# Optimization experiments

Hardware: AMD Instinct MI355X
Metric: run time of the kernel (lower is better)

Reference implementation:

```python
import jax, jax.numpy as jnp
import numpy as np

N_NODES = 50000
N_EDGES = 800000
NUM_GRAPHS = 64
EPS = 1e-5


def setup_inputs() -> dict:
    key = jax.random.key(0)
    ks = jax.random.split(key, 24)
    d = {}
    d['x'] = jax.random.normal(ks[0], (N_NODES, 128), dtype=jnp.float32)
    d['edge_index'] = jax.random.randint(ks[1], (2, N_EDGES), 0, N_NODES, dtype=jnp.int32)
    d['batch'] = jnp.sort(jax.random.randint(ks[2], (N_NODES,), 0, NUM_GRAPHS, dtype=jnp.int32))
    def w(k, shape, fan_in):
        return jax.random.normal(k, shape, dtype=jnp.float32) * (1.0 / np.sqrt(fan_in))
    d['W1'] = w(ks[3], (128, 256), 128)
    d['asrc1'] = w(ks[4], (4, 64), 64)
    d['adst1'] = w(ks[5], (4, 64), 64)
    d['b1'] = jnp.zeros((256,), jnp.float32)
    d['g1'] = jnp.ones((256,), jnp.float32)
    d['be1'] = jnp.zeros((256,), jnp.float32)
    d['W2'] = w(ks[6], (256, 256), 256)
    d['asrc2'] = w(ks[7], (4, 64), 64)
    d['adst2'] = w(ks[8], (4, 64), 64)
    d['b2'] = jnp.zeros((256,), jnp.float32)
    d['g2'] = jnp.ones((256,), jnp.float32)
    d['be2'] = jnp.zeros((256,), jnp.float32)
    d['W3'] = w(ks[9], (256, 128), 256)
    d['asrc3'] = w(ks[10], (1, 128), 128)
    d['adst3'] = w(ks[11], (1, 128), 128)
    d['b3'] = jnp.zeros((128,), jnp.float32)
    d['g3'] = jnp.ones((128,), jnp.float32)
    d['be3'] = jnp.zeros((128,), jnp.float32)
    d['Wp'] = w(ks[12], (256, 128), 256)
    d['bp'] = jnp.zeros((128,), jnp.float32)
    return d


def _gat(x, src, dst, W, a_src, a_dst, b, concat):
    # PyG GATConv: shared linear, per-edge additive attention, segment softmax over dst
    N = x.shape[0]
    H, C = a_src.shape
    xl = (x @ W).reshape(N, H, C)                       # [N,H,C]
    a_l = jnp.sum(xl * a_src[None], axis=-1)            # [N,H]
    a_r = jnp.sum(xl * a_dst[None], axis=-1)            # [N,H]
    e = jax.nn.leaky_relu(a_l[src] + a_r[dst], 0.2)     # [E,H]
    m = jax.ops.segment_max(e, dst, num_segments=N)
    m = jnp.where(jnp.isfinite(m), m, 0.0)
    p = jnp.exp(e - m[dst])
    s = jax.ops.segment_sum(p, dst, num_segments=N)
    alpha = p / (s[dst] + 1e-16)                        # [E,H]
    out = jax.ops.segment_sum(alpha[:, :, None] * xl[src], dst, num_segments=N)  # [N,H,C]
    out = out.reshape(N, H * C) if concat else out.mean(axis=1)
    return out + b


def _ln(x, g, b):
    mu = x.mean(-1, keepdims=True)
    var = x.var(-1, keepdims=True)
    return (x - mu) * jax.lax.rsqrt(var + EPS) * g + b


def reference(x, edge_index, batch, W1, asrc1, adst1, b1, g1, be1,
              W2, asrc2, adst2, b2, g2, be2,
              W3, asrc3, adst3, b3, g3, be3, Wp, bp):
    N = x.shape[0]
    loops = jnp.arange(N, dtype=edge_index.dtype)
    src = jnp.concatenate([edge_index[0], loops])  # add_self_loops=True
    dst = jnp.concatenate([edge_index[1], loops])
    h = jax.nn.relu(_ln(_gat(x, src, dst, W1, asrc1, adst1, b1, True), g1, be1))
    h = jax.nn.relu(_ln(_gat(h, src, dst, W2, asrc2, adst2, b2, True), g2, be2))
    h = jax.nn.relu(_ln(_gat(h, src, dst, W3, asrc3, adst3, b3, False), g3, be3))
    cnt = jax.ops.segment_sum(jnp.ones((N,), h.dtype), batch, num_segments=NUM_GRAPHS)
    h_mean = jax.ops.segment_sum(h, batch, num_segments=NUM_GRAPHS) / jnp.maximum(cnt, 1.0)[:, None]
    h_max = jax.ops.segment_max(h, batch, num_segments=NUM_GRAPHS)
    g = jnp.concatenate([h_mean, h_max], axis=-1)       # [B, 2*embed]
    return g @ Wp + bp
```

## Files before the change

kernel.cpp:

```cpp
#include <hip/hip_runtime.h>

#define EPS_LN 1e-5f
typedef unsigned int uint;

using bf16x8 = __attribute__((ext_vector_type(8))) short;
using f32x4  = __attribute__((ext_vector_type(4))) float;

__device__ inline float bf2f(ushort h){ return __uint_as_float(((uint)h) << 16); }
__device__ inline ushort f2bf(float f){
  uint u = __float_as_uint(f);
  u += 0x7fffu + ((u >> 16) & 1u);
  return (ushort)(u >> 16);
}

__device__ inline void gload_lds16(const ushort* g, ushort* l){
  __builtin_amdgcn_global_load_lds(
      (const __attribute__((address_space(1))) uint*)g,
      (__attribute__((address_space(3))) uint*)l, 16, 0, 0);
}

#define POOL_Q 32

__global__ void k_deg(const int* __restrict__ ei, int* __restrict__ deg, int E, int N){
  int e = blockIdx.x * 256 + threadIdx.x;
  if (e >= E + N) return;
  int dst = (e < E) ? ei[E + e] : (e - E);
  atomicAdd(&deg[dst], 1);
}

__global__ __launch_bounds__(1024) void k_bsum(const int* __restrict__ deg, int* __restrict__ bsum, int n){
  __shared__ int ws[16];
  const int t = (int)threadIdx.x, lane = t & 63, w = t >> 6;
  int i = blockIdx.x * 1024 + t;
  int v = (i < n) ? deg[i] : 0;
  #pragma unroll
  for (int off = 32; off; off >>= 1) v += __shfl_xor(v, off);
  if (lane == 0) ws[w] = v;
  __syncthreads();
  if (t == 0){
    int s = 0;
    #pragma unroll
    for (int k = 0; k < 16; k++) s += ws[k];
    bsum[blockIdx.x] = s;
  }
}

__global__ __launch_bounds__(256) void k_misc(int* __restrict__ bsum, int nb,
                                              const int* __restrict__ batch, int* __restrict__ pos,
                                              float* __restrict__ pool_sum, uint* __restrict__ pool_max,
                                              int N, int G){
  const int t = (int)threadIdx.x;
  const int b = (int)blockIdx.x;
  if (b == 0){
    if (t >= 64) return;
    const int lane = t;
    int carry = 0;
    for (int b0 = 0; b0 < nb; b0 += 64){
      int i = b0 + lane;
      int v = (i < nb) ? bsum[i] : 0;
      int s = v;
      #pragma unroll
      for (int off = 1; off < 64; off <<= 1){ int u = __shfl_up(s, off); if (lane >= off) s += u; }
      if (i < nb) bsum[i] = s - v + carry;
      carry += __shfl(s, 63);
    }
  } else if (b == 1){
    int g = t;
    if (g > G) return;
    int lo = 0, hi = N;
    while (lo < hi){
      int mid = (lo + hi) >> 1;
      if (batch[mid] < g) lo = mid + 1; else hi = mid;
    }
    pos[g] = lo;
  } else {
    int i = (b - 2) * 256 + t;
    if (i < G * 128){ pool_sum[i] = 0.f; pool_max[i] = 0u; }
  }
}

__global__ __launch_bounds__(1024) void k_scan2(const int* __restrict__ deg, const int* __restrict__ bpre,
                                                int* __restrict__ row_ptr, int* __restrict__ cursor, int n){
  __shared__ int wsum[16];
  const int t = (int)threadIdx.x, lane = t & 63, w = t >> 6;
  int i = blockIdx.x * 1024 + t;
  int v = (i < n) ? deg[i] : 0;
  int s = v;
  #pragma unroll
  for (int off = 1; off < 64; off <<= 1){ int u = __shfl_up(s, off); if (lane >= off) s += u; }
  if (lane == 63) wsum[w] = s;
  __syncthreads();
  if (w == 0 && lane < 16){
    int sc = wsum[lane];
    #pragma unroll
    for (int off = 1; off < 16; off <<= 1){ int u = __shfl_up(sc, off); if (lane >= off) sc += u; }
    wsum[lane] = sc;
  }
  __syncthreads();
  int prefix = bpre[blockIdx.x] + (w ? wsum[w - 1] : 0) + s;
  if (i < n){ row_ptr[i + 1] = prefix; cursor[i] = prefix - v; }
  if (i == 0) row_ptr[0] = 0;
}

__global__ void k_scatter(const int* __restrict__ ei, int* __restrict__ cursor,
                          int* __restrict__ csr_src, int E, int N){
  int e = blockIdx.x * 256 + threadIdx.x;
  if (e >= E + N) return;
  int src, dst;
  if (e < E){ src = ei[e]; dst = ei[E + e]; } else { src = dst = e - E; }
  int pos = atomicAdd(&cursor[dst], 1);
  csr_src[pos] = src;
}

__global__ void k_prep(const float* __restrict__ x, ushort* __restrict__ x_bf,
                       const float* __restrict__ W1, ushort* __restrict__ W1t,
                       const float* __restrict__ W2, ushort* __restrict__ W2t,
                       const float* __restrict__ W3, ushort* __restrict__ W3t, int N){
  int i = blockIdx.x * 256 + threadIdx.x;
  const int c0 = N * 32;
  if (i < c0){
    float4 v = reinterpret_cast<const float4*>(x)[i];
    ushort4 o; o.x = f2bf(v.x); o.y = f2bf(v.y); o.z = f2bf(v.z); o.w = f2bf(v.w);
    reinterpret_cast<ushort4*>(x_bf)[i] = o;
    return;
  }
  i -= c0;
  if (i < 256 * 128){
    int n = i >> 7, k = i & 127;
    W1t[i] = f2bf(W1[(size_t)k * 256 + n]);
    return;
  }
  i -= 256 * 128;
  if (i < 256 * 256){
    int n = i >> 8, k = i & 255;
    W2t[i] = f2bf(W2[(size_t)k * 256 + n]);
    return;
  }
  i -= 256 * 256;
  if (i < 128 * 256){
    int n = i >> 8, k = i & 255;
    W3t[i] = f2bf(W3[(size_t)k * 128 + n]);
  }
}

template<int K, int N, int H>
__global__ __launch_bounds__(256, 4) void k_mm(const ushort* __restrict__ A,
                                               const ushort* __restrict__ Wt,
                                               ushort* __restrict__ out,
                                               const float* __restrict__ asrc,
                                               const float* __restrict__ adst,
                                               float* __restrict__ al, float* __restrict__ ar,
                                               int M)
{
  constexpr int BANDS = (N / H) / 64;
  __shared__ __align__(16) ushort ldsA[128 * 64];
  __shared__ __align__(16) ushort ldsB[128 * 64];

  const int t = (int)threadIdx.x;
  const int lane = t & 63;
  const int w = t >> 6;
  const int wm = w >> 1, wn = w & 1;
  const int row0 = blockIdx.x * 128;
  const int n0 = blockIdx.y * 128;
  const int growR = w * 8 + (lane >> 3);
  const int gcolA = (lane & 7) * 8;

  f32x4 acc[4][4];
  #pragma unroll
  for (int mt = 0; mt < 4; mt++)
    #pragma unroll
    for (int nt = 0; nt < 4; nt++)
      acc[mt][nt] = (f32x4){0.f, 0.f, 0.f, 0.f};

  #pragma unroll
  for (int kt = 0; kt < K / 64; kt++){
    if (kt) __syncthreads();
    #pragma unroll
    for (int r = 0; r < 4; r++){
      int ga = row0 + r * 32 + growR; if (ga > M - 1) ga = M - 1;
      int gb = n0 + r * 32 + growR;
      gload_lds16(&A [(size_t)ga * K + kt * 64 + gcolA], ldsA + r * 2048 + w * 512);
      gload_lds16(&Wt[(size_t)gb * K + kt * 64 + gcolA], ldsB + r * 2048 + w * 512);
    }
    __syncthreads();

    #pragma unroll
    for (int ks = 0; ks < 2; ks++){
      bf16x8 af[4], bfr[4];
      const int kb8 = ks * 4 + (lane >> 4);
      #pragma unroll
      for (int mt = 0; mt < 4; mt++){
        int arow = wm * 64 + mt * 16 + (lane & 15);
        af[mt]  = *reinterpret_cast<const bf16x8*>(&ldsA[arow * 64 + kb8 * 8]);
        int brow = wn * 64 + mt * 16 + (lane & 15);
        bfr[mt] = *reinterpret_cast<const bf16x8*>(&ldsB[brow * 64 + kb8 * 8]);
      }
      #pragma unroll
      for (int mt = 0; mt < 4; mt++)
        #pragma unroll
        for (int nt = 0; nt < 4; nt++)
          acc[mt][nt] = __builtin_amdgcn_mfma_f32_16x16x32_bf16(af[mt], bfr[nt], acc[mt][nt], 0, 0, 0);
    }
  }

  #pragma unroll
  for (int mt = 0; mt < 4; mt++){
    const int grow_b = row0 + wm * 64 + mt * 16 + (lane >> 4) * 4;
    #pragma unroll
    for (int nt = 0; nt < 4; nt++){
      const int gcol = n0 + wn * 64 + nt * 16 + (lane & 15);
      #pragma unroll
      for (int r = 0; r < 4; r++){
        int grow = grow_b + r;
        if (grow < M) out[(size_t)grow * N + gcol] = f2bf(acc[mt][nt][r]);
      }
    }
  }

  float av[4], bv[4];
  #pragma unroll
  for (int nt = 0; nt < 4; nt++){
    int col = n0 + wn * 64 + nt * 16 + (lane & 15);
    av[nt] = asrc[col]; bv[nt] = adst[col];
  }
  float paA[4][4], pbA[4][4];
  #pragma unroll
  for (int mt = 0; mt < 4; mt++){
    #pragma unroll
    for (int r = 0; r < 4; r++){
      float pa = acc[mt][0][r] * av[0] + acc[mt][1][r] * av[1]
               + acc[mt][2][r] * av[2] + acc[mt][3][r] * av[3];
      float pb = acc[mt][0][r] * bv[0] + acc[mt][1][r] * bv[1]
               + acc[mt][2][r] * bv[2] + acc[mt][3][r] * bv[3];
      #pragma unroll
      for (int off = 1; off < 16; off <<= 1){ pa += __shfl_xor(pa, off); pb += __shfl_xor(pb, off); }
      paA[mt][r] = pa; pbA[mt][r] = pb;
    }
  }
  if constexpr (BANDS == 1){
    const int h = (n0 + wn * 64) / (N / H);
    if ((lane & 15) == 0){
      #pragma unroll
      for (int mt = 0; mt < 4; mt++){
        #pragma unroll
        for (int r = 0; r < 4; r++){
          int row = row0 + wm * 64 + mt * 16 + (lane >> 4) * 4 + r;
          if (row < M){
            al[(size_t)row * H + h] = paA[mt][r];
            ar[(size_t)row * H + h] = pbA[mt][r];
          }
        }
      }
    }
  } else {
    __syncthreads();
    float* fl = reinterpret_cast<float*>(ldsA);
    if (wn == 0 && (lane & 15) == 0){
      #pragma unroll
      for (int mt = 0; mt < 4; mt++){
        #pragma unroll
        for (int r = 0; r < 4; r++){
          int rl = wm * 64 + mt * 16 + (lane >> 4) * 4 + r;
          fl[rl] = paA[mt][r]; fl[128 + rl] = pbA[mt][r];
        }
      }
    }
    __syncthreads();
    if (wn == 1 && (lane & 15) == 0){
      #pragma unroll
      for (int mt = 0; mt < 4; mt++){
        #pragma unroll
        for (int r = 0; r < 4; r++){
          int rl = wm * 64 + mt * 16 + (lane >> 4) * 4 + r;
          int row = row0 + rl;
          if (row < M){
            al[row] = fl[rl] + paA[mt][r];
            ar[row] = fl[128 + rl] + pbA[mt][r];
          }
        }
      }
    }
  }
}

template<int DIM>
__device__ inline void gstep4(const char* __restrict__ xlb, int laneB, int s, float p, float* acc){
  uint2 v = *reinterpret_cast<const uint2*>(xlb + (size_t)((uint)s * (uint)(DIM * 2)) + laneB);
  acc[0] = fmaf(p, __uint_as_float(v.x << 16), acc[0]);
  acc[1] = fmaf(p, __uint_as_float(v.x & 0xffff0000u), acc[1]);
  acc[2] = fmaf(p, __uint_as_float(v.y << 16), acc[2]);
  acc[3] = fmaf(p, __uint_as_float(v.y & 0xffff0000u), acc[3]);
}
template<int DIM>
__device__ inline void gstep2(const char* __restrict__ xlb, int laneB, int s, float p, float* acc){
  uint v = *reinterpret_cast<const uint*>(xlb + (size_t)((uint)s * (uint)(DIM * 2)) + laneB);
  acc[0] = fmaf(p, __uint_as_float(v << 16), acc[0]);
  acc[1] = fmaf(p, __uint_as_float(v & 0xffff0000u), acc[1]);
}

template<int H, int DIM, bool BF16_OUT>
__global__ __launch_bounds__(256) void k_aggw(
    const ushort* __restrict__ xl,
    const float* __restrict__ al, const float* __restrict__ ar,
    const int* __restrict__ row_ptr, const int* __restrict__ csr_src,
    const float* __restrict__ bias, const float* __restrict__ gamma, const float* __restrict__ beta,
    float* __restrict__ out, int N)
{
  constexpr int EPL = DIM / 64;
  constexpr int PST = 68;
  const int tid = (int)threadIdx.x;
  const int wid = tid >> 6, lane = tid & 63;
  __shared__ float plds_all[4][H * PST];
  __shared__ int   slds_all[4][64];
  float* plds = plds_all[wid];
  int*   slds = slds_all[wid];
  const int n = blockIdx.x * 4 + wid;
  if (n >= N) return;
  const int start = __builtin_amdgcn_readfirstlane(row_ptr[n]);
  const int end   = __builtin_amdgcn_readfirstlane(row_ptr[n + 1]);
  const int deg   = end - start;
  const int hm    = (H == 4) ? (lane >> 4) : 0;
  const int hb    = hm * PST;
  const int laneB = lane * (EPL * 2);

  float arv[H];
  #pragma unroll
  for (int h = 0; h < H; h++) arv[h] = ar[(size_t)n * H + h];

  float acc[EPL];
  #pragma unroll
  for (int e = 0; e < EPL; e++) acc[e] = 0.f;
  float psum[H];
  const char* xlb = (const char*)xl;

  auto gather = [&](int cnt){
    int j = 0;
    for (; j + 8 <= cnt; j += 8){
      int s0 = slds[j+0], s1 = slds[j+1], s2 = slds[j+2], s3 = slds[j+3];
      int s4 = slds[j+4], s5 = slds[j+5], s6 = slds[j+6], s7 = slds[j+7];
      float q0 = plds[hb+j+0], q1 = plds[hb+j+1], q2 = plds[hb+j+2], q3 = plds[hb+j+3];
      float q4 = plds[hb+j+4], q5 = plds[hb+j+5], q6 = plds[hb+j+6], q7 = plds[hb+j+7];
      if constexpr (EPL == 4){
        gstep4<DIM>(xlb, laneB, s0, q0, acc); gstep4<DIM>(xlb, laneB, s1, q1, acc);
        gstep4<DIM>(xlb, laneB, s2, q2, acc); gstep4<DIM>(xlb, laneB, s3, q3, acc);
        gstep4<DIM>(xlb, laneB, s4, q4, acc); gstep4<DIM>(xlb, laneB, s5, q5, acc);
        gstep4<DIM>(xlb, laneB, s6, q6, acc); gstep4<DIM>(xlb, laneB, s7, q7, acc);
      } else {
        gstep2<DIM>(xlb, laneB, s0, q0, acc); gstep2<DIM>(xlb, laneB, s1, q1, acc);
        gstep2<DIM>(xlb, laneB, s2, q2, acc); gstep2<DIM>(xlb, laneB, s3, q3, acc);
        gstep2<DIM>(xlb, laneB, s4, q4, acc); gstep2<DIM>(xlb, laneB, s5, q5, acc);
        gstep2<DIM>(xlb, laneB, s6, q6, acc); gstep2<DIM>(xlb, laneB, s7, q7, acc);
      }
    }
    for (; j + 2 <= cnt; j += 2){
      int s0 = slds[j+0], s1 = slds[j+1];
      float q0 = plds[hb+j+0], q1 = plds[hb+j+1];
      if constexpr (EPL == 4){ gstep4<DIM>(xlb, laneB, s0, q0, acc); gstep4<DIM>(xlb, laneB, s1, q1, acc); }
      else                   { gstep2<DIM>(xlb, laneB, s0, q0, acc); gstep2<DIM>(xlb, laneB, s1, q1, acc); }
    }
    if (j < cnt){
      int s0 = slds[j];
      float q0 = plds[hb+j];
      if constexpr (EPL == 4) gstep4<DIM>(xlb, laneB, s0, q0, acc);
      else                    gstep2<DIM>(xlb, laneB, s0, q0, acc);
    }
  };

  if (deg <= 64){
    int src = csr_src[start + (lane < deg ? lane : deg - 1)];
    slds[lane] = src;
    float e[H];
    if constexpr (H == 4){
      float4 a4 = *reinterpret_cast<const float4*>(&al[(size_t)src * 4]);
      e[0] = a4.x + arv[0]; e[1] = a4.y + arv[1]; e[2] = a4.z + arv[2]; e[3] = a4.w + arv[3];
    } else {
      e[0] = al[src] + arv[0];
    }
    #pragma unroll
    for (int h = 0; h < H; h++){
      e[h] = e[h] > 0.f ? e[h] : 0.2f * e[h];
      if (lane >= deg) e[h] = -1e30f;
    }
    float mx[H];
    #pragma unroll
    for (int h = 0; h < H; h++){
      mx[h] = e[h];
      #pragma unroll
      for (int off = 32; off; off >>= 1) mx[h] = fmaxf(mx[h], __shfl_xor(mx[h], off));
    }
    #pragma unroll
    for (int h = 0; h < H; h++){
      float p = (lane < deg) ? __expf(e[h] - mx[h]) : 0.f;
      plds[h * PST + lane] = p;
      psum[h] = p;
      #pragma unroll
      for (int off = 32; off; off >>= 1) psum[h] += __shfl_xor(psum[h], off);
    }
    __asm__ volatile("s_waitcnt lgkmcnt(0)" ::: "memory");
    __builtin_amdgcn_wave_barrier();
    gather(deg);
  } else {
    float mx[H];
    #pragma unroll
    for (int h = 0; h < H; h++) mx[h] = -1e30f;
    for (int i = start + lane; i < end; i += 64){
      int src = csr_src[i];
      if constexpr (H == 4){
        float4 a4 = *reinterpret_cast<const float4*>(&al[(size_t)src * 4]);
        float e0 = a4.x + arv[0]; e0 = e0 > 0.f ? e0 : 0.2f * e0; mx[0] = fmaxf(mx[0], e0);
        float e1 = a4.y + arv[1]; e1 = e1 > 0.f ? e1 : 0.2f * e1; mx[1] = fmaxf(mx[1], e1);
        float e2 = a4.z + arv[2]; e2 = e2 > 0.f ? e2 : 0.2f * e2; mx[2] = fmaxf(mx[2], e2);
        float e3 = a4.w + arv[3]; e3 = e3 > 0.f ? e3 : 0.2f * e3; mx[3] = fmaxf(mx[3], e3);
      } else {
        float e = al[src] + arv[0]; e = e > 0.f ? e : 0.2f * e; mx[0] = fmaxf(mx[0], e);
      }
    }
    #pragma unroll
    for (int h = 0; h < H; h++){
      #pragma unroll
      for (int off = 32; off; off >>= 1) mx[h] = fmaxf(mx[h], __shfl_xor(mx[h], off));
    }
    #pragma unroll
    for (int h = 0; h < H; h++) psum[h] = 0.f;
    for (int c0 = start; c0 < end; c0 += 64){
      const int cnt = min(64, end - c0);
      __asm__ volatile("s_waitcnt lgkmcnt(0)" ::: "memory");
      __builtin_amdgcn_wave_barrier();
      if (lane < cnt){
        int src = csr_src[c0 + lane];
        slds[lane] = src;
        if constexpr (H == 4){
          float4 a4 = *reinterpret_cast<const float4*>(&al[(size_t)src * 4]);
          float e0 = a4.x + arv[0]; e0 = e0 > 0.f ? e0 : 0.2f * e0; float p0 = __expf(e0 - mx[0]);
          float e1 = a4.y + arv[1]; e1 = e1 > 0.f ? e1 : 0.2f * e1; float p1 = __expf(e1 - mx[1]);
          float e2 = a4.z + arv[2]; e2 = e2 > 0.f ? e2 : 0.2f * e2; float p2 = __expf(e2 - mx[2]);
          float e3 = a4.w + arv[3]; e3 = e3 > 0.f ? e3 : 0.2f * e3; float p3 = __expf(e3 - mx[3]);
          plds[0 * PST + lane] = p0; plds[1 * PST + lane] = p1;
          plds[2 * PST + lane] = p2; plds[3 * PST + lane] = p3;
          psum[0] += p0; psum[1] += p1; psum[2] += p2; psum[3] += p3;
        } else {
          float e = al[src] + arv[0]; e = e > 0.f ? e : 0.2f * e; float p = __expf(e - mx[0]);
          plds[lane] = p; psum[0] += p;
        }
      }
      __asm__ volatile("s_waitcnt lgkmcnt(0)" ::: "memory");
      __builtin_amdgcn_wave_barrier();
      gather(cnt);
    }
    #pragma unroll
    for (int h = 0; h < H; h++){
      #pragma unroll
      for (int off = 32; off; off >>= 1) psum[h] += __shfl_xor(psum[h], off);
    }
  }

  float ssel;
  if constexpr (H == 4){
    ssel = (hm == 0) ? psum[0] : (hm == 1) ? psum[1] : (hm == 2) ? psum[2] : psum[3];
  } else {
    ssel = psum[0];
  }
  const float inv = 1.f / (ssel + 1e-16f);

  float v[EPL];
  if constexpr (EPL == 4){
    float4 bb = *reinterpret_cast<const float4*>(&bias[lane * 4]);
    v[0] = fmaf(acc[0], inv, bb.x); v[1] = fmaf(acc[1], inv, bb.y);
    v[2] = fmaf(acc[2], inv, bb.z); v[3] = fmaf(acc[3], inv, bb.w);
  } else {
    float2 bb = *reinterpret_cast<const float2*>(&bias[lane * 2]);
    v[0] = fmaf(acc[0], inv, bb.x); v[1] = fmaf(acc[1], inv, bb.y);
  }
  float s1 = 0.f, s2 = 0.f;
  #pragma unroll
  for (int e = 0; e < EPL; e++){ s1 += v[e]; s2 += v[e] * v[e]; }
  #pragma unroll
  for (int off = 32; off; off >>= 1){ s1 += __shfl_xor(s1, off); s2 += __shfl_xor(s2, off); }
  const float mu = s1 / DIM;
  const float rstd = rsqrtf(s2 / DIM - mu * mu + EPS_LN);

  if constexpr (EPL == 4){
    float4 gg = *reinterpret_cast<const float4*>(&gamma[lane * 4]);
    float4 be = *reinterpret_cast<const float4*>(&beta[lane * 4]);
    float o0 = fmaxf((v[0] - mu) * rstd * gg.x + be.x, 0.f);
    float o1 = fmaxf((v[1] - mu) * rstd * gg.y + be.y, 0.f);
    float o2 = fmaxf((v[2] - mu) * rstd * gg.z + be.z, 0.f);
    float o3 = fmaxf((v[3] - mu) * rstd * gg.w + be.w, 0.f);
    if constexpr (BF16_OUT){
      uint2 pk;
      pk.x = (uint)f2bf(o0) | ((uint)f2bf(o1) << 16);
      pk.y = (uint)f2bf(o2) | ((uint)f2bf(o3) << 16);
      *reinterpret_cast<uint2*>(&reinterpret_cast<ushort*>(out)[(size_t)n * DIM + lane * 4]) = pk;
    } else {
      *reinterpret_cast<float4*>(&out[(size_t)n * DIM + lane * 4]) = make_float4(o0, o1, o2, o3);
    }
  } else {
    float2 gg = *reinterpret_cast<const float2*>(&gamma[lane * 2]);
    float2 be = *reinterpret_cast<const float2*>(&beta[lane * 2]);
    float o0 = fmaxf((v[0] - mu) * rstd * gg.x + be.x, 0.f);
    float o1 = fmaxf((v[1] - mu) * rstd * gg.y + be.y, 0.f);
    if constexpr (BF16_OUT){
      uint pk = (uint)f2bf(o0) | ((uint)f2bf(o1) << 16);
      reinterpret_cast<uint*>(out)[(size_t)n * (DIM / 2) + lane] = pk;
    } else {
      *reinterpret_cast<float2*>(&out[(size_t)n * DIM + lane * 2]) = make_float2(o0, o1);
    }
  }
}

__global__ __launch_bounds__(256) void k_pool(const float* __restrict__ h, const int* __restrict__ pos,
    float* __restrict__ pool_sum, uint* __restrict__ pool_max){
  const int t = (int)threadIdx.x;
  const int g = blockIdx.x / POOL_Q;
  const int q = blockIdx.x % POOL_Q;
  const int s = pos[g], e = pos[g + 1];
  const int len = e - s;
  if (len <= 0) return;
  const int chunk = (len + POOL_Q - 1) / POOL_Q;
  const int n0 = s + q * chunk;
  const int n1 = min(n0 + chunk, e);
  if (n0 >= n1) return;
  const int qd = t & 31;
  const int slot = t >> 5;
  const int wid = t >> 6;

  float4 sum = make_float4(0.f, 0.f, 0.f, 0.f);
  float4 mx  = make_float4(0.f, 0.f, 0.f, 0.f);
  for (int n = n0 + slot; n < n1; n += 8){
    float4 v = *reinterpret_cast<const float4*>(&h[(size_t)n * 128 + qd * 4]);
    sum.x += v.x; sum.y += v.y; sum.z += v.z; sum.w += v.w;
    mx.x = fmaxf(mx.x, v.x); mx.y = fmaxf(mx.y, v.y);
    mx.z = fmaxf(mx.z, v.z); mx.w = fmaxf(mx.w, v.w);
  }
  sum.x += __shfl_xor(sum.x, 32); sum.y += __shfl_xor(sum.y, 32);
  sum.z += __shfl_xor(sum.z, 32); sum.w += __shfl_xor(sum.w, 32);
  mx.x = fmaxf(mx.x, __shfl_xor(mx.x, 32)); mx.y = fmaxf(mx.y, __shfl_xor(mx.y, 32));
  mx.z = fmaxf(mx.z, __shfl_xor(mx.z, 32)); mx.w = fmaxf(mx.w, __shfl_xor(mx.w, 32));
  __shared__ float4 lsum[4][32], lmax[4][32];
  if ((t & 63) < 32){ lsum[wid][qd] = sum; lmax[wid][qd] = mx; }
  __syncthreads();
  if (t < 32){
    float4 S = lsum[0][t], M = lmax[0][t];
    #pragma unroll
    for (int w = 1; w < 4; w++){
      float4 S2 = lsum[w][t], M2 = lmax[w][t];
      S.x += S2.x; S.y += S2.y; S.z += S2.z; S.w += S2.w;
      M.x = fmaxf(M.x, M2.x); M.y = fmaxf(M.y, M2.y);
      M.z = fmaxf(M.z, M2.z); M.w = fmaxf(M.w, M2.w);
    }
    float* ps = &pool_sum[g * 128 + t * 4];
    uint*  pm = &pool_max[g * 128 + t * 4];
    atomicAdd(&ps[0], S.x); atomicAdd(&ps[1], S.y);
    atomicAdd(&ps[2], S.z); atomicAdd(&ps[3], S.w);
    atomicMax(&pm[0], __float_as_uint(M.x)); atomicMax(&pm[1], __float_as_uint(M.y));
    atomicMax(&pm[2], __float_as_uint(M.z)); atomicMax(&pm[3], __float_as_uint(M.w));
  }
}

__global__ __launch_bounds__(128) void k_final(const float* __restrict__ pool_sum,
    const uint* __restrict__ pool_max, const int* __restrict__ pos,
    const float* __restrict__ Wp, const float* __restrict__ bp, float* __restrict__ out){
  const int g = blockIdx.x;
  const int j = (int)threadIdx.x;
  float inv = 1.f / fmaxf((float)(pos[g + 1] - pos[g]), 1.f);
  float acc = bp[j];
  #pragma unroll 4
  for (int k = 0; k < 128; k++)
    acc = fmaf(pool_sum[g * 128 + k] * inv, Wp[k * 128 + j], acc);
  #pragma unroll 4
  for (int k = 0; k < 128; k++)
    acc = fmaf(__uint_as_float(pool_max[g * 128 + k]), Wp[(128 + k) * 128 + j], acc);
  out[g * 128 + j] = acc;
}

extern "C" void kernel_launch(void* const* d_in, const int* in_sizes, int n_in,
                              void* d_out, int out_size, void* d_ws, size_t ws_size,
                              hipStream_t stream){
  const float* x     = (const float*)d_in[0];
  const int*   ei    = (const int*)d_in[1];
  const int*   batch = (const int*)d_in[2];
  const float* W1    = (const float*)d_in[3];
  const float* asrc1 = (const float*)d_in[4];
  const float* adst1 = (const float*)d_in[5];
  const float* b1    = (const float*)d_in[6];
  const float* g1    = (const float*)d_in[7];
  const float* be1   = (const float*)d_in[8];
  const float* W2    = (const float*)d_in[9];
  const float* asrc2 = (const float*)d_in[10];
  const float* adst2 = (const float*)d_in[11];
  const float* b2    = (const float*)d_in[12];
  const float* g2    = (const float*)d_in[13];
  const float* be2   = (const float*)d_in[14];
  const float* W3    = (const float*)d_in[15];
  const float* asrc3 = (const float*)d_in[16];
  const float* adst3 = (const float*)d_in[17];
  const float* b3    = (const float*)d_in[18];
  const float* g3    = (const float*)d_in[19];
  const float* be3   = (const float*)d_in[20];
  const float* Wp    = (const float*)d_in[21];
  const float* bp    = (const float*)d_in[22];

  const int N = in_sizes[0] / 128;
  const int E = in_sizes[1] / 2;
  const int G = out_size / 128;
  const int EN = E + N;

  char* ws = (char*)d_ws;
  size_t off = 0;
  auto alloc = [&](size_t bytes) -> char* {
    char* p = ws + off;
    off = (off + bytes + 255) & ~(size_t)255;
    return p;
  };
  ushort*   region0  = (ushort*)alloc((size_t)N * 256 * 2);
  ushort*   x_bf     = region0;
  ushort*   h_bf     = region0;
  ushort*   xbufA    = (ushort*)alloc((size_t)N * 256 * 2);
  float*    xbufB    = (float*)alloc((size_t)N * 128 * 4);
  float*    al       = (float*)alloc((size_t)N * 4 * 4);
  float*    ar       = (float*)alloc((size_t)N * 4 * 4);
  int*      deg      = (int*)alloc((size_t)N * 4);
  int*      row_ptr  = (int*)alloc((size_t)(N + 1) * 4);
  int*      cursor   = (int*)alloc((size_t)N * 4);
  int*      csr_src  = (int*)alloc((size_t)EN * 4);
  int*      pos      = (int*)alloc((size_t)(G + 1) * 4);
  float*    pool_sum = (float*)alloc((size_t)G * 128 * 4);
  uint*     pool_max = (uint*)alloc((size_t)G * 128 * 4);
  ushort*   W1t      = (ushort*)alloc((size_t)256 * 128 * 2);
  ushort*   W2t      = (ushort*)alloc((size_t)256 * 256 * 2);
  ushort*   W3t      = (ushort*)alloc((size_t)128 * 256 * 2);
  const int NB = (N + 1023) / 1024;
  int*      bsum     = (int*)alloc((size_t)NB * 4);

  hipMemsetAsync(deg, 0, (size_t)N * 4, stream);

  k_deg<<<(EN + 255) / 256, 256, 0, stream>>>(ei, deg, E, N);
  k_bsum<<<NB, 1024, 0, stream>>>(deg, bsum, N);
  k_misc<<<2 + (G * 128 + 255) / 256, 256, 0, stream>>>(bsum, NB, batch, pos, pool_sum, pool_max, N, G);
  k_scan2<<<NB, 1024, 0, stream>>>(deg, bsum, row_ptr, cursor, N);
  k_scatter<<<(EN + 255) / 256, 256, 0, stream>>>(ei, cursor, csr_src, E, N);
  {
    int total = N * 32 + 256 * 128 + 256 * 256 + 128 * 256;
    k_prep<<<(total + 255) / 256, 256, 0, stream>>>(x, x_bf, W1, W1t, W2, W2t, W3, W3t, N);
  }

  const int MB = (N + 127) / 128;
  const int NB4 = (N + 3) / 4;

  k_mm<128, 256, 4><<<dim3(MB, 2), 256, 0, stream>>>(x_bf, W1t, xbufA, asrc1, adst1, al, ar, N);
  k_aggw<4, 256, true><<<NB4, 256, 0, stream>>>(xbufA, al, ar, row_ptr, csr_src, b1, g1, be1, (float*)h_bf, N);

  k_mm<256, 256, 4><<<dim3(MB, 2), 256, 0, stream>>>(h_bf, W2t, xbufA, asrc2, adst2, al, ar, N);
  k_aggw<4, 256, true><<<NB4, 256, 0, stream>>>(xbufA, al, ar, row_ptr, csr_src, b2, g2, be2, (float*)h_bf, N);

  k_mm<256, 128, 1><<<dim3(MB, 1), 256, 0, stream>>>(h_bf, W3t, xbufA, asrc3, adst3, al, ar, N);
  k_aggw<1, 128, false><<<NB4, 256, 0, stream>>>(xbufA, al, ar, row_ptr, csr_src, b3, g3, be3, xbufB, N);

  k_pool<<<G * POOL_Q, 256, 0, stream>>>(xbufB, pos, pool_sum, pool_max);
  k_final<<<G, 128, 0, stream>>>(pool_sum, pool_max, pos, Wp, bp, (float*)d_out);
}
```

Before: 380.0 us.

## Use 512-thread full-width GEMM tiles and fold degree counting into prep kernel

Adds a k_mm8 kernel in which one 512-thread block computes all 256 output columns for 128 rows. The A tile is loaded once instead of once per column-half block, and each wave writes its head's attention logits directly. The degree atomics move into k_prep, which removes one kernel launch. Costs are higher LDS use per block (48 KB), lower occupancy, and atomic traffic mixed into the conversion kernel.

```diff
diff --git a/kernel.cpp b/kernel.cpp
--- a/kernel.cpp
+++ b/kernel.cpp
@@ -20,13 +20,6 @@
 }
 
 #define POOL_Q 32
-
-__global__ void k_deg(const int* __restrict__ ei, int* __restrict__ deg, int E, int N){
-  int e = blockIdx.x * 256 + threadIdx.x;
-  if (e >= E + N) return;
-  int dst = (e < E) ? ei[E + e] : (e - E);
-  atomicAdd(&deg[dst], 1);
-}
 
 __global__ __launch_bounds__(1024) void k_bsum(const int* __restrict__ deg, int* __restrict__ bsum, int n){
   __shared__ int ws[16];
@@ -115,7 +108,9 @@
 __global__ void k_prep(const float* __restrict__ x, ushort* __restrict__ x_bf,
                        const float* __restrict__ W1, ushort* __restrict__ W1t,
                        const float* __restrict__ W2, ushort* __restrict__ W2t,
-                       const float* __restrict__ W3, ushort* __restrict__ W3t, int N){
+                       const float* __restrict__ W3, ushort* __restrict__ W3t,
+                       const int* __restrict__ ei, int* __restrict__ deg,
+                       int N, int E){
   int i = blockIdx.x * 256 + threadIdx.x;
   const int c0 = N * 32;
   if (i < c0){
@@ -140,6 +135,114 @@
   if (i < 128 * 256){
     int n = i >> 8, k = i & 255;
     W3t[i] = f2bf(W3[(size_t)k * 128 + n]);
+    return;
+  }
+  i -= 128 * 256;
+  if (i < E + N){
+    int dst = (i < E) ? ei[E + i] : (i - E);
+    atomicAdd(&deg[dst], 1);
+  }
+}
+
+template<int K>
+__global__ __launch_bounds__(512, 2) void k_mm8(const ushort* __restrict__ A,
+                                                const ushort* __restrict__ Wt,
+                                                ushort* __restrict__ out,
+                                                const float* __restrict__ asrc,
+                                                const float* __restrict__ adst,
+                                                float* __restrict__ al, float* __restrict__ ar,
+                                                int M)
+{
+  __shared__ __align__(16) ushort ldsA[128 * 64];
+  __shared__ __align__(16) ushort ldsB[256 * 64];
+
+  const int t = (int)threadIdx.x;
+  const int lane = t & 63;
+  const int w = t >> 6;
+  const int wm = w >> 2, wn = w & 3;
+  const int row0 = blockIdx.x * 128;
+  const int rr = t >> 3;
+  const int gcolA = (t & 7) * 8;
+
+  f32x4 acc[4][4];
+  #pragma unroll
+  for (int mt = 0; mt < 4; mt++)
+    #pragma unroll
+    for (int nt = 0; nt < 4; nt++)
+      acc[mt][nt] = (f32x4){0.f, 0.f, 0.f, 0.f};
+
+  #pragma unroll
+  for (int kt = 0; kt < K / 64; kt++){
+    if (kt) __syncthreads();
+    #pragma unroll
+    for (int r = 0; r < 2; r++){
+      int ga = row0 + r * 64 + rr; if (ga > M - 1) ga = M - 1;
+      gload_lds16(&A[(size_t)ga * K + kt * 64 + gcolA], ldsA + r * 4096 + w * 512);
+    }
+    #pragma unroll
+    for (int r = 0; r < 4; r++){
+      int gb = r * 64 + rr;
+      gload_lds16(&Wt[(size_t)gb * K + kt * 64 + gcolA], ldsB + r * 4096 + w * 512);
+    }
+    __syncthreads();
+
+    #pragma unroll
+    for (int ks = 0; ks < 2; ks++){
+      bf16x8 af[4], bfr[4];
+      const int kb8 = ks * 4 + (lane >> 4);
+      #pragma unroll
+      for (int mt = 0; mt < 4; mt++){
+        int arow = wm * 64 + mt * 16 + (lane & 15);
+        af[mt]  = *reinterpret_cast<const bf16x8*>(&ldsA[arow * 64 + kb8 * 8]);
+        int brow = wn * 64 + mt * 16 + (lane & 15);
+        bfr[mt] = *reinterpret_cast<const bf16x8*>(&ldsB[brow * 64 + kb8 * 8]);
+      }
+      #pragma unroll
+      for (int mt = 0; mt < 4; mt++)
+        #pragma unroll
+        for (int nt = 0; nt < 4; nt++)
+          acc[mt][nt] = __builtin_amdgcn_mfma_f32_16x16x32_bf16(af[mt], bfr[nt], acc[mt][nt], 0, 0, 0);
+    }
+  }
+
+  #pragma unroll
+  for (int mt = 0; mt < 4; mt++){
+    const int grow_b = row0 + wm * 64 + mt * 16 + (lane >> 4) * 4;
+    #pragma unroll
+    for (int nt = 0; nt < 4; nt++){
+      const int gcol = wn * 64 + nt * 16 + (lane & 15);
+      #pragma unroll
+      for (int r = 0; r < 4; r++){
+        int grow = grow_b + r;
+        if (grow < M) out[(size_t)grow * 256 + gcol] = f2bf(acc[mt][nt][r]);
+      }
+    }
+  }
+
+  float av[4], bv[4];
+  #pragma unroll
+  for (int nt = 0; nt < 4; nt++){
+    int col = wn * 64 + nt * 16 + (lane & 15);
+    av[nt] = asrc[col]; bv[nt] = adst[col];
+  }
+  #pragma unroll
+  for (int mt = 0; mt < 4; mt++){
+    #pragma unroll
+    for (int r = 0; r < 4; r++){
+      float pa = acc[mt][0][r] * av[0] + acc[mt][1][r] * av[1]
+               + acc[mt][2][r] * av[2] + acc[mt][3][r] * av[3];
+      float pb = acc[mt][0][r] * bv[0] + acc[mt][1][r] * bv[1]
+               + acc[mt][2][r] * bv[2] + acc[mt][3][r] * bv[3];
+      #pragma unroll
+      for (int off = 1; off < 16; off <<= 1){ pa += __shfl_xor(pa, off); pb += __shfl_xor(pb, off); }
+      if ((lane & 15) == 0){
+        int row = row0 + wm * 64 + mt * 16 + (lane >> 4) * 4 + r;
+        if (row < M){
+          al[(size_t)row * 4 + wn] = pa;
+          ar[(size_t)row * 4 + wn] = pb;
+        }
+      }
+    }
   }
 }
 
@@ -152,7 +255,6 @@
                                                float* __restrict__ al, float* __restrict__ ar,
                                                int M)
 {
-  constexpr int BANDS = (N / H) / 64;
   __shared__ __align__(16) ushort ldsA[128 * 64];
   __shared__ __align__(16) ushort ldsB[128 * 64];
 
@@ -161,7 +263,6 @@
   const int w = t >> 6;
   const int wm = w >> 1, wn = w & 1;
   const int row0 = blockIdx.x * 128;
-  const int n0 = blockIdx.y * 128;
   const int growR = w * 8 + (lane >> 3);
   const int gcolA = (lane & 7) * 8;
 
@@ -178,7 +279,7 @@
     #pragma unroll
     for (int r = 0; r < 4; r++){
       int ga = row0 + r * 32 + growR; if (ga > M - 1) ga = M - 1;
-      int gb = n0 + r * 32 + growR;
+      int gb = r * 32 + growR;
       gload_lds16(&A [(size_t)ga * K + kt * 64 + gcolA], ldsA + r * 2048 + w * 512);
       gload_lds16(&Wt[(size_t)gb * K + kt * 64 + gcolA], ldsB + r * 2048 + w * 512);
     }
@@ -208,7 +309,7 @@
     const int grow_b = row0 + wm * 64 + mt * 16 + (lane >> 4) * 4;
     #pragma unroll
     for (int nt = 0; nt < 4; nt++){
-      const int gcol = n0 + wn * 64 + nt * 16 + (lane & 15);
+      const int gcol = wn * 64 + nt * 16 + (lane & 15);
       #pragma unroll
       for (int r = 0; r < 4; r++){
         int grow = grow_b + r;
@@ -220,7 +321,7 @@
   float av[4], bv[4];
   #pragma unroll
   for (int nt = 0; nt < 4; nt++){
-    int col = n0 + wn * 64 + nt * 16 + (lane & 15);
+    int col = wn * 64 + nt * 16 + (lane & 15);
     av[nt] = asrc[col]; bv[nt] = adst[col];
   }
   float paA[4][4], pbA[4][4];
@@ -237,46 +338,29 @@
       paA[mt][r] = pa; pbA[mt][r] = pb;
     }
   }
-  if constexpr (BANDS == 1){
-    const int h = (n0 + wn * 64) / (N / H);
-    if ((lane & 15) == 0){
-      #pragma unroll
-      for (int mt = 0; mt < 4; mt++){
-        #pragma unroll
-        for (int r = 0; r < 4; r++){
-          int row = row0 + wm * 64 + mt * 16 + (lane >> 4) * 4 + r;
-          if (row < M){
-            al[(size_t)row * H + h] = paA[mt][r];
-            ar[(size_t)row * H + h] = pbA[mt][r];
-          }
-        }
-      }
-    }
-  } else {
-    __syncthreads();
-    float* fl = reinterpret_cast<float*>(ldsA);
-    if (wn == 0 && (lane & 15) == 0){
-      #pragma unroll
-      for (int mt = 0; mt < 4; mt++){
-        #pragma unroll
-        for (int r = 0; r < 4; r++){
-          int rl = wm * 64 + mt * 16 + (lane >> 4) * 4 + r;
-          fl[rl] = paA[mt][r]; fl[128 + rl] = pbA[mt][r];
-        }
-      }
-    }
-    __syncthreads();
-    if (wn == 1 && (lane & 15) == 0){
-      #pragma unroll
-      for (int mt = 0; mt < 4; mt++){
-        #pragma unroll
-        for (int r = 0; r < 4; r++){
-          int rl = wm * 64 + mt * 16 + (lane >> 4) * 4 + r;
-          int row = row0 + rl;
-          if (row < M){
-            al[row] = fl[rl] + paA[mt][r];
-            ar[row] = fl[128 + rl] + pbA[mt][r];
-          }
+  __syncthreads();
+  float* fl = reinterpret_cast<float*>(ldsA);
+  if (wn == 0 && (lane & 15) == 0){
+    #pragma unroll
+    for (int mt = 0; mt < 4; mt++){
+      #pragma unroll
+      for (int r = 0; r < 4; r++){
+        int rl = wm * 64 + mt * 16 + (lane >> 4) * 4 + r;
+        fl[rl] = paA[mt][r]; fl[128 + rl] = pbA[mt][r];
+      }
+    }
+  }
+  __syncthreads();
+  if (wn == 1 && (lane & 15) == 0){
+    #pragma unroll
+    for (int mt = 0; mt < 4; mt++){
+      #pragma unroll
+      for (int r = 0; r < 4; r++){
+        int rl = wm * 64 + mt * 16 + (lane >> 4) * 4 + r;
+        int row = row0 + rl;
+        if (row < M){
+          al[row] = fl[rl] + paA[mt][r];
+          ar[row] = fl[128 + rl] + pbA[mt][r];
         }
       }
     }
@@ -634,26 +718,25 @@
 
   hipMemsetAsync(deg, 0, (size_t)N * 4, stream);
 
-  k_deg<<<(EN + 255) / 256, 256, 0, stream>>>(ei, deg, E, N);
+  {
+    int total = N * 32 + 256 * 128 + 256 * 256 + 128 * 256 + EN;
+    k_prep<<<(total + 255) / 256, 256, 0, stream>>>(x, x_bf, W1, W1t, W2, W2t, W3, W3t, ei, deg, N, E);
+  }
   k_bsum<<<NB, 1024, 0, stream>>>(deg, bsum, N);
   k_misc<<<2 + (G * 128 + 255) / 256, 256, 0, stream>>>(bsum, NB, batch, pos, pool_sum, pool_max, N, G);
   k_scan2<<<NB, 1024, 0, stream>>>(deg, bsum, row_ptr, cursor, N);
   k_scatter<<<(EN + 255) / 256, 256, 0, stream>>>(ei, cursor, csr_src, E, N);
-  {
-    int total = N * 32 + 256 * 128 + 256 * 256 + 128 * 256;
-    k_prep<<<(total + 255) / 256, 256, 0, stream>>>(x, x_bf, W1, W1t, W2, W2t, W3, W3t, N);
-  }
 
   const int MB = (N + 127) / 128;
   const int NB4 = (N + 3) / 4;
 
-  k_mm<128, 256, 4><<<dim3(MB, 2), 256, 0, stream>>>(x_bf, W1t, xbufA, asrc1, adst1, al, ar, N);
+  k_mm8<128><<<MB, 512, 0, stream>>>(x_bf, W1t, xbufA, asrc1, adst1, al, ar, N);
   k_aggw<4, 256, true><<<NB4, 256, 0, stream>>>(xbufA, al, ar, row_ptr, csr_src, b1, g1, be1, (float*)h_bf, N);
 
-  k_mm<256, 256, 4><<<dim3(MB, 2), 256, 0, stream>>>(h_bf, W2t, xbufA, asrc2, adst2, al, ar, N);
+  k_mm8<256><<<MB, 512, 0, stream>>>(h_bf, W2t, xbufA, asrc2, adst2, al, ar, N);
   k_aggw<4, 256, true><<<NB4, 256, 0, stream>>>(xbufA, al, ar, row_ptr, csr_src, b2, g2, be2, (float*)h_bf, N);
 
-  k_mm<256, 128, 1><<<dim3(MB, 1), 256, 0, stream>>>(h_bf, W3t, xbufA, asrc3, adst3, al, ar, N);
+  k_mm<256, 128, 1><<<MB, 256, 0, stream>>>(h_bf, W3t, xbufA, asrc3, adst3, al, ar, N);
   k_aggw<1, 128, false><<<NB4, 256, 0, stream>>>(xbufA, al, ar, row_ptr, csr_src, b3, g3, be3, xbufB, N);
 
   k_pool<<<G * POOL_Q, 256, 0, stream>>>(xbufB, pos, pool_sum, pool_max);
```

Measured after the change: 386.2 us. No clear change (+1.6%).
